# Kernel tuning notes

Hardware: AMD Instinct MI355X
Metric: run time of the kernel (lower is better)

The kernel has to match this reference:

```python
import jax, jax.numpy as jnp
import numpy as np

N, T, V, C_IN = 32, 300, 25, 64
K, F = 3, 128  # spatial kernel size, output filters


def setup_inputs() -> dict:
    key = jax.random.key(0)
    k1, k2, k3, k4 = jax.random.split(key, 4)
    x = jax.random.normal(k1, (N, T, V, C_IN), dtype=jnp.float32)
    A = jax.random.uniform(k2, (K, V, V), dtype=jnp.float32)
    # Conv2D kernel (t_kernel_size=1, 1, C_in, F*K), HWIO layout
    W = jax.random.normal(k3, (1, 1, C_IN, F * K), dtype=jnp.float32) * (1.0 / np.sqrt(C_IN))
    b = jax.random.normal(k4, (F * K,), dtype=jnp.float32) * 0.01
    return {"x": x, "A": A, "W": W, "b": b}


def reference(x, A, W, b):
    # Conv2D with (1,1) kernel == pointwise channel mixing: (N,T,V,Cin) @ (Cin, F*K)
    h = jnp.einsum('ntvc,cd->ntvd', x, W[0, 0]) + b  # (N, T, V, F*K)
    # Reshape channel dim into (K, F): matches Keras Reshape([t, v, K, c//K])
    h = h.reshape(N, T, V, K, F)
    # Graph aggregation over the K-partition adjacency: ntvkc, kvw -> ntwc
    y = jnp.einsum('ntvkc,kvw->ntwc', h, A)  # (N, T, V, F)
    return y
```

## Files before the change

kernel.cpp:

```cpp
#include <hip/hip_runtime.h>

#define N_ 32
#define T_ 300
#define V_ 25
#define C_ 64
#define F_ 128
#define K_ 3
#define D_ 384
#define TB 2
#define NBLK (N_ * (T_ / TB))

typedef _Float16 f16;
typedef f16  f16x4v __attribute__((ext_vector_type(4)));
typedef f16  f16x8v __attribute__((ext_vector_type(8)));
typedef float f32x4v __attribute__((ext_vector_type(4)));

#define WS_WT 0
#define WS_A2 49152

__global__ void gcn_prep(const float* __restrict__ A, const float* __restrict__ W,
                         f16* __restrict__ Wt, f16* __restrict__ A2) {
    int tid = blockIdx.x * blockDim.x + threadIdx.x;
    if (tid < D_ * C_) {
        int d = tid >> 6, c = tid & 63;
        Wt[tid] = (f16)W[c * D_ + d];
    }
    int t2 = tid - D_ * C_;
    if (t2 >= 0 && t2 < K_ * 32 * 32) {
        int k = t2 >> 10, r = t2 & 1023, w = r >> 5, v = r & 31;
        float val = (w < V_ && v < V_) ? A[(k * V_ + v) * V_ + w] : 0.0f;
        A2[t2] = (f16)val;
    }
}

__global__ __launch_bounds__(256, 4) void gcn_fused(
    const float* __restrict__ x, const f16* __restrict__ Wt,
    const f16* __restrict__ A2g, const float* __restrict__ b,
    float* __restrict__ y)
{
    __shared__ __align__(16) f16 x_lds[64][72];
    __shared__ __align__(16) f16 hT_lds[128 * 64];

    const int tid  = threadIdx.x;
    const int lane = tid & 63;
    const int wave = tid >> 6;
    const int l15  = lane & 15;
    const int lgr  = lane >> 4;
    const int koff = lgr * 8;

    const int n  = blockIdx.x / (T_ / TB);
    const int t0 = (blockIdx.x % (T_ / TB)) * TB;

    {
        const float4* xs = (const float4*)(x + ((size_t)n * T_ + t0) * (V_ * C_));
        #pragma unroll
        for (int i = 0; i < 4; ++i) {
            int idx = tid + i * 256;
            if (idx < TB * V_ * C_ / 4) {
                float4 v4 = xs[idx];
                int e = idx * 4;
                int t = e / (V_ * C_);
                int r = e - t * (V_ * C_);
                int v = r >> 6, c = r & 63;
                f16x4v hv;
                hv[0] = (f16)v4.x; hv[1] = (f16)v4.y; hv[2] = (f16)v4.z; hv[3] = (f16)v4.w;
                *(f16x4v*)&x_lds[t * 32 + v][c] = hv;
            }
        }
    }
    if (tid < TB * 7 * C_ / 4) {
        int e = tid * 4;
        int t = e / (7 * C_);
        int r = e - t * (7 * C_);
        int v = 25 + (r >> 6), c = r & 63;
        f16x4v z = {(f16)0.f, (f16)0.f, (f16)0.f, (f16)0.f};
        *(f16x4v*)&x_lds[t * 32 + v][c] = z;
    }

    float bias[K_][2];
    #pragma unroll
    for (int k = 0; k < K_; ++k)
        #pragma unroll
        for (int nt = 0; nt < 2; ++nt)
            bias[k][nt] = b[k * F_ + wave * 32 + nt * 16 + l15];

    f32x4v zero4 = {0.f, 0.f, 0.f, 0.f};
    f32x4v acc2[2][4];
    #pragma unroll
    for (int mt = 0; mt < 2; ++mt)
        #pragma unroll
        for (int nt = 0; nt < 4; ++nt)
            acc2[mt][nt] = zero4;

    const int t  = wave >> 1;
    const int nh = (wave & 1) * 4;
    const f16* wrow = Wt + (size_t)(wave * 32 + l15) * C_ + koff;

    __syncthreads();

    #pragma unroll
    for (int k = 0; k < K_; ++k) {
        if (k) __syncthreads();

        f16x8v wfr[2][2];
        #pragma unroll
        for (int nt = 0; nt < 2; ++nt)
            #pragma unroll
            for (int kt = 0; kt < 2; ++kt)
                wfr[nt][kt] = *(const f16x8v*)(wrow + (size_t)(k * F_ + nt * 16) * C_ + kt * 32);

        {
            f16x8v xa[4][2];
            #pragma unroll
            for (int mt = 0; mt < 4; ++mt) {
                const f16* xr = &x_lds[mt * 16 + l15][koff];
                xa[mt][0] = *(const f16x8v*)(xr);
                xa[mt][1] = *(const f16x8v*)(xr + 32);
            }
            f32x4v acc1[4][2];
            #pragma unroll
            for (int mt = 0; mt < 4; ++mt)
                #pragma unroll
                for (int nt = 0; nt < 2; ++nt)
                    acc1[mt][nt] = zero4;
            #pragma unroll
            for (int kt = 0; kt < 2; ++kt)
                #pragma unroll
                for (int mt = 0; mt < 4; ++mt)
                    #pragma unroll
                    for (int nt = 0; nt < 2; ++nt)
                        acc1[mt][nt] = __builtin_amdgcn_mfma_f32_16x16x32_f16(
                            xa[mt][kt], wfr[nt][kt], acc1[mt][nt], 0, 0, 0);
            char* hb = (char*)hT_lds;
            #pragma unroll
            for (int mt = 0; mt < 4; ++mt)
                #pragma unroll
                for (int nt = 0; nt < 2; ++nt) {
                    int d = wave * 32 + nt * 16 + l15;
                    float bv = bias[k][nt];
                    f16x4v h4;
                    #pragma unroll
                    for (int r = 0; r < 4; ++r) h4[r] = (f16)(acc1[mt][nt][r] + bv);
                    int off = (d * 128 + (mt * 16 + lgr * 4) * 2) ^ ((d & 7) << 4);
                    *(f16x4v*)(hb + off) = h4;
                }
        }

        f16x8v a2f[2];
        #pragma unroll
        for (int mt = 0; mt < 2; ++mt)
            a2f[mt] = *(const f16x8v*)(A2g + ((size_t)(k * 32 + mt * 16 + l15) * 32 + koff));

        __syncthreads();

        {
            const char* hb = (const char*)hT_lds;
            #pragma unroll
            for (int nt = 0; nt < 4; ++nt) {
                int f = (nh + nt) * 16 + l15;
                int off = (f * 128 + (t * 32 + koff) * 2) ^ ((f & 7) << 4);
                f16x8v bv = *(const f16x8v*)(hb + off);
                #pragma unroll
                for (int mt = 0; mt < 2; ++mt)
                    acc2[mt][nt] = __builtin_amdgcn_mfma_f32_16x16x32_f16(
                        a2f[mt], bv, acc2[mt][nt], 0, 0, 0);
            }
        }
    }

    {
        float* yr = y + (((size_t)n * T_ + (t0 + t)) * V_) * F_;
        #pragma unroll
        for (int mt = 0; mt < 2; ++mt) {
            int wb = mt * 16 + lgr * 4;
            #pragma unroll
            for (int nt = 0; nt < 4; ++nt) {
                int f = (nh + nt) * 16 + l15;
                #pragma unroll
                for (int r = 0; r < 4; ++r) {
                    int w = wb + r;
                    if (w < V_) {
                        yr[(size_t)w * F_ + f] = acc2[mt][nt][r];
                    }
                }
            }
        }
    }
}

extern "C" void kernel_launch(void* const* d_in, const int* in_sizes, int n_in,
                              void* d_out, int out_size, void* d_ws, size_t ws_size,
                              hipStream_t stream) {
    const float* x = (const float*)d_in[0];
    const float* A = (const float*)d_in[1];
    const float* W = (const float*)d_in[2];
    const float* b = (const float*)d_in[3];
    float* yout = (float*)d_out;

    f16* Wt = (f16*)((char*)d_ws + WS_WT);
    f16* A2 = (f16*)((char*)d_ws + WS_A2);

    const int prep_threads = D_ * C_ + K_ * 32 * 32;
    gcn_prep<<<(prep_threads + 255) / 256, 256, 0, stream>>>(A, W, Wt, A2);
    gcn_fused<<<NBLK, 256, 0, stream>>>(x, Wt, A2, b, yout);
}
```

Baseline: 65.43 us.

## Assign one timestep per wave with private LDS tiles, removing block barriers

Restructures the fused kernel so that each wave independently handles one (n,t) timestep. It loads x straight from global into MFMA fragments, stages h in a per-wave LDS tile, and runs the graph aggregation with swapped operands so the output is stored as float4 rows. This removes the block-wide __syncthreads and the shared x staging, and makes the output writes vectorized. In exchange, each wave now reloads the full W slice from global/L2 per k, and occupancy is lowered to 3 blocks per SIMD.

Measured after the change: 102.5 us. 1.57x slower.

```diff
diff --git a/kernel.cpp b/kernel.cpp
--- a/kernel.cpp
+++ b/kernel.cpp
@@ -6,9 +6,8 @@
 #define C_ 64
 #define F_ 128
 #define K_ 3
-#define D_ 384
-#define TB 2
-#define NBLK (N_ * (T_ / TB))
+#define NT_ (N_ * T_)
+#define NBLK (NT_ / 4)
 
 typedef _Float16 f16;
 typedef f16  f16x4v __attribute__((ext_vector_type(4)));
@@ -21,11 +20,11 @@
 __global__ void gcn_prep(const float* __restrict__ A, const float* __restrict__ W,
                          f16* __restrict__ Wt, f16* __restrict__ A2) {
     int tid = blockIdx.x * blockDim.x + threadIdx.x;
-    if (tid < D_ * C_) {
+    if (tid < K_ * F_ * C_) {
         int d = tid >> 6, c = tid & 63;
-        Wt[tid] = (f16)W[c * D_ + d];
+        Wt[tid] = (f16)W[c * (K_ * F_) + d];
     }
-    int t2 = tid - D_ * C_;
+    int t2 = tid - K_ * F_ * C_;
     if (t2 >= 0 && t2 < K_ * 32 * 32) {
         int k = t2 >> 10, r = t2 & 1023, w = r >> 5, v = r & 31;
         float val = (w < V_ && v < V_) ? A[(k * V_ + v) * V_ + w] : 0.0f;
@@ -33,13 +32,12 @@
     }
 }
 
-__global__ __launch_bounds__(256, 4) void gcn_fused(
+__global__ __launch_bounds__(256, 3) void gcn_fused(
     const float* __restrict__ x, const f16* __restrict__ Wt,
     const f16* __restrict__ A2g, const float* __restrict__ b,
     float* __restrict__ y)
 {
-    __shared__ __align__(16) f16 x_lds[64][72];
-    __shared__ __align__(16) f16 hT_lds[128 * 64];
+    __shared__ __align__(16) char tb_all[4][128 * 80];
 
     const int tid  = threadIdx.x;
     const int lane = tid & 63;
@@ -48,140 +46,106 @@
     const int lgr  = lane >> 4;
     const int koff = lgr * 8;
 
-    const int n  = blockIdx.x / (T_ / TB);
-    const int t0 = (blockIdx.x % (T_ / TB)) * TB;
+    char* tb = tb_all[wave];
 
-    {
-        const float4* xs = (const float4*)(x + ((size_t)n * T_ + t0) * (V_ * C_));
+    const int gid = blockIdx.x * 4 + wave;
+    const int n = gid / T_, t = gid % T_;
+    const float* xt = x + ((size_t)n * T_ + t) * (V_ * C_);
+
+    f16x8v xf[2][2];
+    #pragma unroll
+    for (int nt2 = 0; nt2 < 2; ++nt2) {
+        const int v = nt2 * 16 + l15;
+        const bool ok = (v < V_);
         #pragma unroll
-        for (int i = 0; i < 4; ++i) {
-            int idx = tid + i * 256;
-            if (idx < TB * V_ * C_ / 4) {
-                float4 v4 = xs[idx];
-                int e = idx * 4;
-                int t = e / (V_ * C_);
-                int r = e - t * (V_ * C_);
-                int v = r >> 6, c = r & 63;
-                f16x4v hv;
-                hv[0] = (f16)v4.x; hv[1] = (f16)v4.y; hv[2] = (f16)v4.z; hv[3] = (f16)v4.w;
-                *(f16x4v*)&x_lds[t * 32 + v][c] = hv;
+        for (int kt = 0; kt < 2; ++kt) {
+            float4 lo = {0.f, 0.f, 0.f, 0.f}, hi = {0.f, 0.f, 0.f, 0.f};
+            if (ok) {
+                const float4* p = (const float4*)(xt + v * C_ + kt * 32 + koff);
+                lo = p[0]; hi = p[1];
             }
+            f16x8v f;
+            f[0] = (f16)lo.x; f[1] = (f16)lo.y; f[2] = (f16)lo.z; f[3] = (f16)lo.w;
+            f[4] = (f16)hi.x; f[5] = (f16)hi.y; f[6] = (f16)hi.z; f[7] = (f16)hi.w;
+            xf[nt2][kt] = f;
         }
     }
-    if (tid < TB * 7 * C_ / 4) {
-        int e = tid * 4;
-        int t = e / (7 * C_);
-        int r = e - t * (7 * C_);
-        int v = 25 + (r >> 6), c = r & 63;
-        f16x4v z = {(f16)0.f, (f16)0.f, (f16)0.f, (f16)0.f};
-        *(f16x4v*)&x_lds[t * 32 + v][c] = z;
-    }
 
-    float bias[K_][2];
+    f32x4v zero4 = {0.f, 0.f, 0.f, 0.f};
+    f32x4v accy[8][2];
     #pragma unroll
-    for (int k = 0; k < K_; ++k)
+    for (int ft = 0; ft < 8; ++ft)
         #pragma unroll
         for (int nt = 0; nt < 2; ++nt)
-            bias[k][nt] = b[k * F_ + wave * 32 + nt * 16 + l15];
+            accy[ft][nt] = zero4;
 
-    f32x4v zero4 = {0.f, 0.f, 0.f, 0.f};
-    f32x4v acc2[2][4];
-    #pragma unroll
-    for (int mt = 0; mt < 2; ++mt)
-        #pragma unroll
-        for (int nt = 0; nt < 4; ++nt)
-            acc2[mt][nt] = zero4;
-
-    const int t  = wave >> 1;
-    const int nh = (wave & 1) * 4;
-    const f16* wrow = Wt + (size_t)(wave * 32 + l15) * C_ + koff;
-
-    __syncthreads();
-
-    #pragma unroll
+    #pragma unroll 1
     for (int k = 0; k < K_; ++k) {
-        if (k) __syncthreads();
-
-        f16x8v wfr[2][2];
+        f16x8v a2f[2];
         #pragma unroll
         for (int nt = 0; nt < 2; ++nt)
-            #pragma unroll
-            for (int kt = 0; kt < 2; ++kt)
-                wfr[nt][kt] = *(const f16x8v*)(wrow + (size_t)(k * F_ + nt * 16) * C_ + kt * 32);
+            a2f[nt] = *(const f16x8v*)(A2g + (size_t)k * 1024 + (nt * 16 + l15) * 32 + koff);
 
-        {
-            f16x8v xa[4][2];
+        #pragma unroll
+        for (int half = 0; half < 2; ++half) {
+            f16x8v wfr[4][2];
             #pragma unroll
             for (int mt = 0; mt < 4; ++mt) {
-                const f16* xr = &x_lds[mt * 16 + l15][koff];
-                xa[mt][0] = *(const f16x8v*)(xr);
-                xa[mt][1] = *(const f16x8v*)(xr + 32);
+                const int d = k * F_ + (half * 4 + mt) * 16 + l15;
+                #pragma unroll
+                for (int kt = 0; kt < 2; ++kt)
+                    wfr[mt][kt] = *(const f16x8v*)(Wt + (size_t)d * C_ + kt * 32 + koff);
             }
             f32x4v acc1[4][2];
             #pragma unroll
             for (int mt = 0; mt < 4; ++mt)
                 #pragma unroll
-                for (int nt = 0; nt < 2; ++nt)
-                    acc1[mt][nt] = zero4;
+                for (int nt2 = 0; nt2 < 2; ++nt2)
+                    acc1[mt][nt2] = zero4;
             #pragma unroll
             for (int kt = 0; kt < 2; ++kt)
                 #pragma unroll
                 for (int mt = 0; mt < 4; ++mt)
                     #pragma unroll
-                    for (int nt = 0; nt < 2; ++nt)
-                        acc1[mt][nt] = __builtin_amdgcn_mfma_f32_16x16x32_f16(
-                            xa[mt][kt], wfr[nt][kt], acc1[mt][nt], 0, 0, 0);
-            char* hb = (char*)hT_lds;
+                    for (int nt2 = 0; nt2 < 2; ++nt2)
+                        acc1[mt][nt2] = __builtin_amdgcn_mfma_f32_16x16x32_f16(
+                            xf[nt2][kt], wfr[mt][kt], acc1[mt][nt2], 0, 0, 0);
             #pragma unroll
-            for (int mt = 0; mt < 4; ++mt)
+            for (int mt = 0; mt < 4; ++mt) {
+                const int f = (half * 4 + mt) * 16 + l15;
+                const float bv = b[k * F_ + f];
                 #pragma unroll
-                for (int nt = 0; nt < 2; ++nt) {
-                    int d = wave * 32 + nt * 16 + l15;
-                    float bv = bias[k][nt];
+                for (int nt2 = 0; nt2 < 2; ++nt2) {
                     f16x4v h4;
                     #pragma unroll
-                    for (int r = 0; r < 4; ++r) h4[r] = (f16)(acc1[mt][nt][r] + bv);
-                    int off = (d * 128 + (mt * 16 + lgr * 4) * 2) ^ ((d & 7) << 4);
-                    *(f16x4v*)(hb + off) = h4;
+                    for (int r = 0; r < 4; ++r) h4[r] = (f16)(acc1[mt][nt2][r] + bv);
+                    *(f16x4v*)(tb + f * 80 + nt2 * 32 + lgr * 8) = h4;
                 }
+            }
         }
 
-        f16x8v a2f[2];
         #pragma unroll
-        for (int mt = 0; mt < 2; ++mt)
-            a2f[mt] = *(const f16x8v*)(A2g + ((size_t)(k * 32 + mt * 16 + l15) * 32 + koff));
-
-        __syncthreads();
-
-        {
-            const char* hb = (const char*)hT_lds;
+        for (int ft = 0; ft < 8; ++ft) {
+            const f16x8v afr = *(const f16x8v*)(tb + (ft * 16 + l15) * 80 + lgr * 16);
             #pragma unroll
-            for (int nt = 0; nt < 4; ++nt) {
-                int f = (nh + nt) * 16 + l15;
-                int off = (f * 128 + (t * 32 + koff) * 2) ^ ((f & 7) << 4);
-                f16x8v bv = *(const f16x8v*)(hb + off);
-                #pragma unroll
-                for (int mt = 0; mt < 2; ++mt)
-                    acc2[mt][nt] = __builtin_amdgcn_mfma_f32_16x16x32_f16(
-                        a2f[mt], bv, acc2[mt][nt], 0, 0, 0);
-            }
+            for (int nt = 0; nt < 2; ++nt)
+                accy[ft][nt] = __builtin_amdgcn_mfma_f32_16x16x32_f16(
+                    afr, a2f[nt], accy[ft][nt], 0, 0, 0);
         }
     }
 
     {
-        float* yr = y + (((size_t)n * T_ + (t0 + t)) * V_) * F_;
+        float* yt = y + (((size_t)n * T_ + t) * V_) * F_;
         #pragma unroll
-        for (int mt = 0; mt < 2; ++mt) {
-            int wb = mt * 16 + lgr * 4;
-            #pragma unroll
-            for (int nt = 0; nt < 4; ++nt) {
-                int f = (nh + nt) * 16 + l15;
+        for (int nt = 0; nt < 2; ++nt) {
+            const int w = nt * 16 + l15;
+            if (w < V_) {
                 #pragma unroll
-                for (int r = 0; r < 4; ++r) {
-                    int w = wb + r;
-                    if (w < V_) {
-                        yr[(size_t)w * F_ + f] = acc2[mt][nt][r];
-                    }
+                for (int ft = 0; ft < 8; ++ft) {
+                    float4 o;
+                    o.x = accy[ft][nt][0]; o.y = accy[ft][nt][1];
+                    o.z = accy[ft][nt][2]; o.w = accy[ft][nt][3];
+                    *(float4*)(yt + (size_t)w * F_ + ft * 16 + lgr * 4) = o;
                 }
             }
         }
@@ -200,7 +164,7 @@
     f16* Wt = (f16*)((char*)d_ws + WS_WT);
     f16* A2 = (f16*)((char*)d_ws + WS_A2);
 
-    const int prep_threads = D_ * C_ + K_ * 32 * 32;
+    const int prep_threads = K_ * F_ * C_ + K_ * 32 * 32;
     gcn_prep<<<(prep_threads + 255) / 256, 256, 0, stream>>>(A, W, Wt, A2);
     gcn_fused<<<NBLK, 256, 0, stream>>>(x, Wt, A2, b, yout);
 }
```
